# Kernel tuning notes

Measured on AMD Instinct MI355X. Metric: run time of the kernel, lower is better.

## Reference

```python
import jax, jax.numpy as jnp
import numpy as np
from jax import lax

N_CLASS = 21          # VOC: 20 foreground + background
SCORE_THRESH = 0.05   # 'evaluate' preset
NMS_THRESH = 0.3


def loc2bbox(src_bbox, loc):
    # src_bbox, loc: [N, 4] in (y1, x1, y2, x2) / (dy, dx, dh, dw)
    h = src_bbox[:, 2] - src_bbox[:, 0]
    w = src_bbox[:, 3] - src_bbox[:, 1]
    cy = src_bbox[:, 0] + 0.5 * h
    cx = src_bbox[:, 1] + 0.5 * w
    dy, dx, dh, dw = loc[:, 0], loc[:, 1], loc[:, 2], loc[:, 3]
    ncy = dy * h + cy
    ncx = dx * w + cx
    nh = jnp.exp(dh) * h
    nw = jnp.exp(dw) * w
    return jnp.stack([ncy - 0.5 * nh, ncx - 0.5 * nw,
                      ncy + 0.5 * nh, ncx + 0.5 * nw], axis=1)


def pairwise_iou(boxes):
    # boxes: [R, 4] (y1, x1, y2, x2) -> [R, R]
    area = (boxes[:, 2] - boxes[:, 0]) * (boxes[:, 3] - boxes[:, 1])
    ty1 = jnp.maximum(boxes[:, None, 0], boxes[None, :, 0])
    tx1 = jnp.maximum(boxes[:, None, 1], boxes[None, :, 1])
    ty2 = jnp.minimum(boxes[:, None, 2], boxes[None, :, 2])
    tx2 = jnp.minimum(boxes[:, None, 3], boxes[None, :, 3])
    inter = jnp.clip(ty2 - ty1, 0) * jnp.clip(tx2 - tx1, 0)
    union = area[:, None] + area[None, :] - inter
    return inter / jnp.maximum(union, 1e-10)


def nms_keep(boxes, scores):
    # boxes [R,4], scores [R] for one class. Returns bool keep mask [R]
    # (score-thresholded + greedy NMS), fixed shape (mask instead of gather).
    R = boxes.shape[0]
    valid = scores > SCORE_THRESH
    order = jnp.argsort(-scores)
    b = boxes[order]
    v = valid[order]
    suppress = pairwise_iou(b) > NMS_THRESH  # [R, R]
    idx = jnp.arange(R)

    def body(i, keep):
        sup_by_earlier = jnp.any(keep & suppress[:, i] & (idx < i))
        return keep.at[i].set(v[i] & ~sup_by_earlier)

    keep_sorted = lax.fori_loop(0, R, body, jnp.zeros((R,), bool))
    return jnp.zeros((R,), bool).at[order].set(keep_sorted)


def setup_inputs() -> dict:
    key = jax.random.key(0)
    k1, k2, k3, k4 = jax.random.split(key, 4)
    R = 2000
    size_h, size_w = 600, 800
    roi_cls_loc = jax.random.normal(k1, (R, N_CLASS * 4), jnp.float32)
    roi_scores = jax.random.normal(k2, (R, N_CLASS), jnp.float32)
    # valid (y1, x1, y2, x2) rois inside the image
    yx = jax.random.uniform(k3, (R, 2), jnp.float32) * jnp.array([size_h - 32.0, size_w - 32.0])
    hw = 16.0 + jax.random.uniform(k4, (R, 2), jnp.float32) * 128.0
    rois = jnp.concatenate([yx, yx + hw], axis=1)
    return {"roi_cls_loc": roi_cls_loc, "roi_scores": roi_scores,
            "rois": rois, "size_h": size_h, "size_w": size_w}


def reference(roi_cls_loc, roi_scores, rois, size_h, size_w):
    R = rois.shape[0]
    mean = jnp.tile(jnp.asarray([0.0, 0.0, 0.0, 0.0], roi_cls_loc.dtype), N_CLASS)
    std = jnp.tile(jnp.asarray([0.1, 0.1, 0.2, 0.2], roi_cls_loc.dtype), N_CLASS)
    loc = roi_cls_loc * std + mean                      # [R, 4*C]
    loc = loc.reshape(R * N_CLASS, 4)
    src = jnp.broadcast_to(rois[:, None, :], (R, N_CLASS, 4)).reshape(R * N_CLASS, 4)
    box = loc2bbox(src, loc).reshape(R, N_CLASS, 4)
    # clamp y coords (0,2) to [0, H], x coords (1,3) to [0, W]
    y = jnp.clip(box[..., 0::2], 0.0, float(size_h))
    x = jnp.clip(box[..., 1::2], 0.0, float(size_w))
    box = jnp.stack([y[..., 0], x[..., 0], y[..., 1], x[..., 1]], axis=-1)
    prob = jax.nn.softmax(roi_scores, axis=1)           # [R, C]
    # foreground classes only (skip background class 0)
    cls_box = jnp.transpose(box[:, 1:, :], (1, 0, 2))   # [C-1, R, 4]
    cls_prob = prob[:, 1:].T                            # [C-1, R]
    keep = jax.vmap(nms_keep)(lax.stop_gradient(cls_box),
                              lax.stop_gradient(cls_prob))  # [C-1, R] bool
    kept = keep.astype(box.dtype)[..., None]
    # fixed-shape detections: per-class boxes + score, zeroed where suppressed
    out = jnp.concatenate([cls_box * kept, cls_prob[..., None] * kept], axis=-1)
    return out  # [C-1, R, 5]
```

## Files before the change

### kernel.cpp

```cpp
#include <hip/hip_runtime.h>
#include <math.h>

#define NCLS 21
#define NCO 20
#define SUB 8
#define TPB 256
#define RCAP 2048
#define RMAX 2000
#define LDSW 7680
#define SCORE_THRESH 0.05f

typedef unsigned long long u64;
typedef unsigned int u32;
typedef unsigned short u16;

#define IOU_MID (20132661.0 / 67108864.0)

__device__ __forceinline__ u64 readlane64(u64 v, int l) {
    u32 lo = (u32)__builtin_amdgcn_readlane((int)(u32)v, l);
    u32 hi = (u32)__builtin_amdgcn_readlane((int)(u32)(v >> 32), l);
    return ((u64)hi << 32) | lo;
}
__device__ __forceinline__ float readlanef(float v, int l) {
    return __uint_as_float((u32)__builtin_amdgcn_readlane((int)__float_as_uint(v), l));
}
__device__ __forceinline__ u64 shflxor64(u64 v, int m) {
    u32 lo = (u32)__shfl_xor((int)(u32)v, m, 64);
    u32 hi = (u32)__shfl_xor((int)(u32)(v >> 32), m, 64);
    return ((u64)hi << 32) | lo;
}

__device__ __forceinline__ int coff(int ic, int nw) {
    return ((ic * nw - ((ic * (ic - 1)) >> 1)) << 6);
}

__device__ __forceinline__ void decode_box(
    const float* __restrict__ rois, const float* __restrict__ loc,
    int r, int cls, float sh, float sw,
    float& by1, float& bx1, float& by2, float& bx2)
{
    float4 rb = *(const float4*)(rois + r * 4);
    float y1 = rb.x, x1 = rb.y, y2 = rb.z, x2 = rb.w;
    float h = y2 - y1, w = x2 - x1;
    float cy = y1 + 0.5f * h, cx = x1 + 0.5f * w;
    float4 l4 = *(const float4*)(loc + r * (NCLS * 4) + cls * 4);
    float dy = l4.x * 0.1f, dx = l4.y * 0.1f;
    float dh = l4.z * 0.2f, dw = l4.w * 0.2f;
    float ncy = dy * h + cy, ncx = dx * w + cx;
    float nh = expf(dh) * h, nw = expf(dw) * w;
    by1 = fminf(fmaxf(ncy - 0.5f * nh, 0.f), sh);
    bx1 = fminf(fmaxf(ncx - 0.5f * nw, 0.f), sw);
    by2 = fminf(fmaxf(ncy + 0.5f * nh, 0.f), sh);
    bx2 = fminf(fmaxf(ncx + 0.5f * nw, 0.f), sw);
}

__device__ __forceinline__ float softmax_p(
    const float* __restrict__ scores, int r, int cls)
{
    const float* srow = scores + r * NCLS;
    float s[NCLS];
    float4 a0 = *(const float4*)(srow);
    float4 a1 = *(const float4*)(srow + 4);
    float4 a2 = *(const float4*)(srow + 8);
    float4 a3 = *(const float4*)(srow + 12);
    float4 a4 = *(const float4*)(srow + 16);
    s[0]=a0.x; s[1]=a0.y; s[2]=a0.z; s[3]=a0.w;
    s[4]=a1.x; s[5]=a1.y; s[6]=a1.z; s[7]=a1.w;
    s[8]=a2.x; s[9]=a2.y; s[10]=a2.z; s[11]=a2.w;
    s[12]=a3.x; s[13]=a3.y; s[14]=a3.z; s[15]=a3.w;
    s[16]=a4.x; s[17]=a4.y; s[18]=a4.z; s[19]=a4.w;
    s[20]=srow[20];
    float m = -INFINITY;
#pragma unroll
    for (int k = 0; k < NCLS; ++k) m = fmaxf(m, s[k]);
    float sum = 0.f, ec = 0.f;
#pragma unroll
    for (int k = 0; k < NCLS; ++k) {
        float e = expf(s[k] - m);
        sum += e;
        if (k == cls) ec = e;
    }
    return ec / sum;
}

__global__ __launch_bounds__(256) void keygen_kernel(
    const float* __restrict__ scores, u64* __restrict__ ukey,
    int* __restrict__ cntA, int R)
{
    __shared__ u64 lkey[256];
    __shared__ int cnt;
    const int t = threadIdx.x;
    const int c = blockIdx.x >> 3;
    const int s = blockIdx.x & 7;
    const int lane = t & 63;
    if (t == 0) cnt = 0;
    __syncthreads();
    const int rpb = (R + 7) >> 3;
    const int r0 = s * rpb, r1 = min(R, r0 + rpb);
    for (int r = r0 + t; r < r1; r += 256) {
        float p = softmax_p(scores, r, c + 1);
        bool valid = (p > SCORE_THRESH);
        u64 key = ((u64)(~__float_as_uint(p)) << 32) | (u32)r;
        u64 bal = __ballot(valid);
        if (bal) {
            int nb = (int)__popcll(bal);
            int base = 0;
            if (lane == 0) base = atomicAdd(&cnt, nb);
            base = __shfl(base, 0, 64);
            if (valid)
                lkey[base + (int)__popcll(bal & ((1ull << lane) - 1ull))] = key;
        }
    }
    __syncthreads();
    const int n = cnt;
    if (t == 0) cntA[(c << 3) | s] = n;
    for (int j = t; j < n; j += 256)
        ukey[((size_t)c << 11) + (s << 8) + j] = lkey[j];
}

__global__ __launch_bounds__(512) void rank_kernel(
    const float* __restrict__ loc, const float* __restrict__ rois,
    const int* __restrict__ ph, const int* __restrict__ pw,
    const u64* __restrict__ ukey, const int* __restrict__ cntA,
    u64* __restrict__ ord, int* __restrict__ nvv,
    float4* __restrict__ pbG, float* __restrict__ arG, int R)
{
    __shared__ __align__(16) u64 vkey[RCAP + 2];
    const int t = threadIdx.x;
    const int c = blockIdx.x >> 3;
    const int s = blockIdx.x & 7;
    const int wv = t >> 6, lane = t & 63;
    int nv = 0, bseg = 0, nseg = 0;
#pragma unroll
    for (int k = 0; k < 8; ++k) {
        int ck = cntA[(c << 3) | k];
        if (k < wv) bseg += ck;
        if (k == wv) nseg = ck;
        nv += ck;
    }
    for (int j = lane; j < nseg; j += 64)
        vkey[bseg + j] = ukey[((size_t)c << 11) + (wv << 8) + j];
    if (t == 0) vkey[nv] = ~0ull;
    __syncthreads();

    const int sl = (nv + 7) >> 3;
    const int i0 = s * sl;
    const int nmy = max(0, min(nv - i0, sl));
    if (t < nmy) {
        u64 kk = vkey[i0 + t];
        int rank = 0;
        const ulonglong2* vk2 = (const ulonglong2*)vkey;
        const int nj2 = (nv + 1) >> 1;
#pragma unroll 8
        for (int j = 0; j < nj2; ++j) {
            ulonglong2 kj = vk2[j];
            rank += (int)(kj.x < kk) + (int)(kj.y < kk);
        }
        const float sh = (float)(*ph), sw = (float)(*pw);
        int r = (int)(u32)kk;
        float b0, b1, b2, b3;
        decode_box(rois, loc, r, c + 1, sh, sw, b0, b1, b2, b3);
        ord[((size_t)c << 11) + rank] = kk;
        pbG[((size_t)c << 11) + rank] = make_float4(b0, b1, b2, b3);
        arG[((size_t)c << 11) + rank] = (b2 - b0) * (b3 - b1);
    }
    if (t == 0 && s == 0) nvv[c] = nv;
}

__global__ __launch_bounds__(512) void maskp_kernel(
    const float4* __restrict__ pbG, const float* __restrict__ arG,
    const int* __restrict__ nvv, u64* __restrict__ M)
{
    __shared__ float4 pb[RCAP];
    __shared__ float ar[RCAP];
    const int t = threadIdx.x;
    const int c = blockIdx.x >> 3;
    const int s = blockIdx.x & 7;
    const int lane = t & 63;
    const int nv = nvv[c];
    const int nw = (nv + 63) >> 6;
    for (int i = t; i < nv; i += 512) {
        pb[i] = pbG[((size_t)c << 11) + i];
        ar[i] = arG[((size_t)c << 11) + i];
    }
    __syncthreads();

    const int wid = (s << 3) | (t >> 6);
    const int ntasks = nw * (nw + 1) / 2;
    u64* Mc = M + ((size_t)c << 16);
    for (int task = wid; task < ntasks; task += SUB * 8) {
        int ic = 0, rm = task;
        while (rm >= nw - ic) { rm -= nw - ic; ++ic; }
        int v = ic + rm;
        int i = (ic << 6) + lane;
        float4 a = pb[i];
        float iarea = ar[i];
        float4 rj = pb[(v << 6) + lane];
        float ja_l = ar[(v << 6) + lane];
        int jcnt = min(64, nv - (v << 6));
        u64 m = 0;
        for (int jj = 0; jj < jcnt; ++jj) {
            float jy1 = readlanef(rj.x, jj);
            float jx1 = readlanef(rj.y, jj);
            float jy2 = readlanef(rj.z, jj);
            float jx2 = readlanef(rj.w, jj);
            float ja  = readlanef(ja_l, jj);
            float ty1 = fmaxf(a.x, jy1);
            float tx1 = fmaxf(a.y, jx1);
            float ty2 = fminf(a.z, jy2);
            float tx2 = fminf(a.w, jx2);
            float inter = fmaxf(ty2 - ty1, 0.f) * fmaxf(tx2 - tx1, 0.f);
            float uni = fmaxf(iarea + ja - inter, 1e-10f);
            if ((double)inter > IOU_MID * (double)uni) m |= 1ull << jj;
        }
        if (v == ic) m &= (lane < 63) ? (~0ull << (lane + 1)) : 0ull;
        int W = nw - ic;
        if (i < nv) Mc[coff(ic, nw) + lane * W + (v - ic)] = m;
    }
}

__global__ __launch_bounds__(TPB) void resolveout_kernel(
    const float* __restrict__ loc, const float* __restrict__ rois,
    const int* __restrict__ ph, const int* __restrict__ pw,
    const u64* __restrict__ ord, const int* __restrict__ nvv,
    const u64* __restrict__ M, float* __restrict__ out, int R)
{
    __shared__ u64 mlds[LDSW];
    __shared__ u64 keptw[32];
    const int t = threadIdx.x;
    const int c = blockIdx.x >> 3;
    const int s = blockIdx.x & 7;
    const int nv = nvv[c];
    const int nw = (nv + 63) >> 6;
    const u64* Mc = M + ((size_t)c << 16);
    const int S = coff(nw, nw);
    const bool lds_ok = (S <= LDSW);
    if (t < 32) keptw[t] = 0;

    if (lds_ok) {
        for (int base = 0; base < S; base += 2048) {
            u64 v[8];
#pragma unroll
            for (int j = 0; j < 8; ++j) {
                int k = base + (j << 8) + t;
                v[j] = (k < S) ? Mc[k] : 0ull;
            }
#pragma unroll
            for (int j = 0; j < 8; ++j) {
                int k = base + (j << 8) + t;
                if (k < S) mlds[k] = v[j];
            }
        }
    }
    __syncthreads();

    if (t < 64) {
        const int lane = t;
        auto core = [&](const auto* B) {
            u64 remreg = 0;
            for (int w = 0; w < nw; ++w) {
                const int W = nw - w;
                const int cb = coff(w, nw);
                int i = (w << 6) + lane;
                u64 cw = (i < nv) ? B[cb + lane * W] : 0ull;
                int remn = nv - (w << 6);
                u64 vb = (remn >= 64) ? ~0ull : ((1ull << remn) - 1ull);
                u64 cand = vb & ~readlane64(remreg, w);
                u64 X = cand;
                if (X) {
                    for (int it = 0; it < 64; ++it) {
                        u64 contrib = ((X >> lane) & 1ull) ? cw : 0ull;
#pragma unroll
                        for (int d = 1; d < 64; d <<= 1)
                            contrib |= shflxor64(contrib, d);
                        bool keep = ((cand >> lane) & 1ull) &&
                                    !((contrib >> lane) & 1ull);
                        u64 Xn = __ballot(keep);
                        if (Xn == X) break;
                        X = Xn;
                    }
                    if (lane == 0) keptw[w] = X;
                    bool lact = (lane > w) && (lane < nw);
                    u64 km = X, acc = 0;
                    while (km) {
                        int bs[8];
#pragma unroll
                        for (int g = 0; g < 8; ++g) {
                            bs[g] = km ? (__ffsll(km) - 1) : -1;
                            if (km) km &= km - 1;
                        }
                        u64 tmp[8];
#pragma unroll
                        for (int g = 0; g < 8; ++g)
                            tmp[g] = (bs[g] >= 0 && lact)
                                ? B[cb + bs[g] * W + (lane - w)] : 0ull;
#pragma unroll
                        for (int g = 0; g < 8; ++g) acc |= tmp[g];
                    }
                    if (lact) remreg |= acc;
                }
            }
        };
        if (lds_ok) core(mlds); else core(Mc);
    }
    __syncthreads();

    const int chunk = (R + 7) >> 3;
    const int r0 = s * chunk;
    const int r1 = min(R, r0 + chunk);
    float* slice = out + (size_t)c * R * 5;
    for (int k = r0 * 5 + t; k < r1 * 5; k += TPB) slice[k] = 0.f;
    __syncthreads();

    const float sh = (float)(*ph), sw = (float)(*pw);
    for (int i = t; i < nv; i += TPB) {
        if ((keptw[i >> 6] >> (i & 63)) & 1ull) {
            u64 key = ord[((size_t)c << 11) + i];
            int r = (int)(u32)key;
            if (r >= r0 && r < r1) {
                float v0, v1, v2, v3;
                decode_box(rois, loc, r, c + 1, sh, sw, v0, v1, v2, v3);
                float* p = slice + (size_t)r * 5;
                p[0] = v0; p[1] = v1; p[2] = v2; p[3] = v3;
                p[4] = __uint_as_float(~(u32)(key >> 32));
            }
        }
    }
}

#define NTH 1024
__global__ __launch_bounds__(NTH) void fused_kernel(
    const float* __restrict__ loc, const float* __restrict__ scores,
    const float* __restrict__ rois, const int* __restrict__ ph,
    const int* __restrict__ pw, float* __restrict__ out, int R)
{
    __shared__ u64 vkey[RMAX];
    __shared__ float2 p1[RMAX], p2[RMAX];
    __shared__ u64 chunk[64 * 33];
    __shared__ u64 rem[32];
    __shared__ int cnt;

    const int t = threadIdx.x;
    const int lane = t & 63;
    const int c = blockIdx.x + 1;
    const float sh = (float)(*ph), sw = (float)(*pw);

    if (t == 0) cnt = 0;
    if (t < 32) rem[t] = 0;
    __syncthreads();

    for (int r = t; r < R; r += NTH) {
        float p = softmax_p(scores, r, c);
        if (p > SCORE_THRESH) {
            int j = atomicAdd(&cnt, 1);
            vkey[j] = ((u64)(~__float_as_uint(p)) << 32) | (u32)r;
        }
    }
    __syncthreads();
    const int nv = cnt;
    const int nw = (nv + 63) >> 6;

    u64 kk0 = 0, kk1 = 0;
    int r0 = 0, r1 = 0;
    bool in0 = (t < nv), in1 = (t + NTH < nv);
    if (in0) kk0 = vkey[t];
    if (in1) kk1 = vkey[t + NTH];
#pragma unroll 8
    for (int i = 0; i < nv; ++i) {
        u64 k = vkey[i];
        r0 += (k < kk0);
        r1 += (k < kk1);
    }
    __syncthreads();

    for (int u = 0; u < 2; ++u) {
        bool act = u ? in1 : in0;
        if (act) {
            u64 kk = u ? kk1 : kk0;
            int rank = u ? r1 : r0;
            int r = (int)(kk & 0xffffffffu);
            float b0, b1, b2, b3;
            decode_box(rois, loc, r, c, sh, sw, b0, b1, b2, b3);
            vkey[rank] = kk;
            p1[rank] = make_float2(b0, b1);
            p2[rank] = make_float2(b2, b3);
        }
    }
    __syncthreads();

    for (int w = 0; w < nw; ++w) {
        int nwr = nw - w;
        u64 remw = rem[w];
        for (int task = t; task < (nwr << 6); task += NTH) {
            int vr = task >> 6, il = task & 63;
            int i = (w << 6) + il;
            u64 m = 0;
            if (i < nv && !((remw >> il) & 1ull)) {
                int v = w + vr;
                u64 rv = rem[v];
                if (~rv != 0ull) {
                    float2 a1 = p1[i], a2 = p2[i];
                    float iarea = (a2.x - a1.x) * (a2.y - a1.y);
                    int j0 = v << 6;
                    int jhi = min(64, nv - j0);
#pragma unroll 4
                    for (int jj = 0; jj < jhi; ++jj) {
                        float2 b1 = p1[j0 + jj], b2 = p2[j0 + jj];
                        float ty1 = fmaxf(a1.x, b1.x);
                        float tx1 = fmaxf(a1.y, b1.y);
                        float ty2 = fminf(a2.x, b2.x);
                        float tx2 = fminf(a2.y, b2.y);
                        float inter = fmaxf(ty2 - ty1, 0.f) * fmaxf(tx2 - tx1, 0.f);
                        float jarea = (b2.x - b1.x) * (b2.y - b1.y);
                        float uni = fmaxf(iarea + jarea - inter, 1e-10f);
                        if ((double)inter > IOU_MID * (double)uni) m |= 1ull << jj;
                    }
                    if (vr == 0)
                        m &= (il < 63) ? (~0ull << (il + 1)) : 0ull;
                }
            }
            chunk[il * 33 + vr] = m;
        }
        __syncthreads();

        u64 cand = chunk[lane * 33];
        u64 cur = rem[w];
        int remn = nv - (w << 6);
        u64 vb = (remn >= 64) ? ~0ull : ((1ull << remn) - 1ull);
        u64 avail = vb & ~cur;
        u64 kept = 0;
        while (avail) {
            int bb = __ffsll(avail) - 1;
            kept |= 1ull << bb;
            cur |= __shfl(cand, bb, 64);
            avail &= ~(cur | (1ull << bb));
        }
        int vr = t & 31, pg = t >> 5;
        if (vr >= 1 && vr < nwr) {
            u64 acc = 0, km = kept;
            int n = 0;
            while (km) {
                int bb = __ffsll(km) - 1;
                km &= km - 1;
                if ((n & 31) == pg) acc |= chunk[bb * 33 + vr];
                ++n;
            }
            if (acc) atomicOr(&rem[w + vr], acc);
        }
        if (t == 0) rem[w] = cur;
        __syncthreads();
    }

    u16* inv = (u16*)chunk;
    for (int r = t; r < R; r += NTH) inv[r] = 0xffffu;
    __syncthreads();
    for (int i = t; i < nv; i += NTH)
        if (!((rem[i >> 6] >> (i & 63)) & 1ull))
            inv[(int)(vkey[i] & 0xffffffffu)] = (u16)i;
    __syncthreads();
    float* slice = out + (size_t)(c - 1) * R * 5;
    for (int r = t; r < R; r += NTH) {
        int i = inv[r];
        float v0 = 0.f, v1 = 0.f, v2 = 0.f, v3 = 0.f, v4 = 0.f;
        if (i != 0xffff) {
            float2 a1 = p1[i], a2 = p2[i];
            v0 = a1.x; v1 = a1.y; v2 = a2.x; v3 = a2.y;
            v4 = __uint_as_float(~(u32)(vkey[i] >> 32));
        }
        float* p = slice + (size_t)r * 5;
        p[0] = v0; p[1] = v1; p[2] = v2; p[3] = v3; p[4] = v4;
    }
}

extern "C" void kernel_launch(void* const* d_in, const int* in_sizes, int n_in,
                              void* d_out, int out_size, void* d_ws, size_t ws_size,
                              hipStream_t stream) {
    const float* loc    = (const float*)d_in[0];
    const float* scores = (const float*)d_in[1];
    const float* rois   = (const float*)d_in[2];
    const int*   ph     = (const int*)d_in[3];
    const int*   pw     = (const int*)d_in[4];
    float* out = (float*)d_out;
    int R = in_sizes[2] / 4;

    size_t needM    = (size_t)NCO * RCAP * 32 * 8;
    size_t needOrd  = (size_t)NCO * RCAP * 8;
    size_t needUkey = (size_t)NCO * RCAP * 8;
    size_t needPbG  = (size_t)NCO * RCAP * 16;
    size_t needArG  = (size_t)NCO * RCAP * 4;
    size_t need     = needM + needOrd + needUkey + needPbG + needArG + 2048;

    if (R <= RCAP && ws_size >= need) {
        char* w     = (char*)d_ws;
        u64* M      = (u64*)w;                               w += needM;
        u64* ordp   = (u64*)w;                               w += needOrd;
        u64* ukey   = (u64*)w;                               w += needUkey;
        float4* pbG = (float4*)w;                            w += needPbG;
        float* arG  = (float*)w;                             w += needArG;
        int* cntA   = (int*)w;                               w += 1024;
        int* nvv    = (int*)w;
        keygen_kernel<<<NCO * SUB, 256, 0, stream>>>(scores, ukey, cntA, R);
        rank_kernel<<<NCO * SUB, 512, 0, stream>>>(loc, rois, ph, pw, ukey,
                                                   cntA, ordp, nvv, pbG, arG, R);
        maskp_kernel<<<NCO * SUB, 512, 0, stream>>>(pbG, arG, nvv, M);
        resolveout_kernel<<<NCO * SUB, TPB, 0, stream>>>(loc, rois, ph, pw,
                                                         ordp, nvv, M, out, R);
    } else if (R <= RMAX) {
        fused_kernel<<<NCO, NTH, 0, stream>>>(loc, scores, rois, ph, pw, out, R);
    }
}
```

Measured before the change: 116.8 us.

## Raise per-class block count to 12 and split rank counting across four lanes

Raises the number of blocks per class from 8 to 12 in all four kernels, generalising segment indexing for keys and counts. The rank kernel now gives each key four threads, each counting over a quarter of the key array, and combines them with xor shuffles, which shortens the serial compare loop. The aim is more parallelism on a GPU with many compute units and less per-thread latency in ranking. The cost is more blocks that each redo the shared-memory loads (LDS fill in maskp, matrix load in resolveout), plus a new R <= 3072 limit on the fast path.

```diff
diff --git a/kernel.cpp b/kernel.cpp
--- a/kernel.cpp
+++ b/kernel.cpp
@@ -3,10 +3,11 @@
 
 #define NCLS 21
 #define NCO 20
-#define SUB 8
+#define SUB 12
 #define TPB 256
 #define RCAP 2048
 #define RMAX 2000
+#define SEGW 256
 #define LDSW 7680
 #define SCORE_THRESH 0.05f
 
@@ -83,21 +84,21 @@
     return ec / sum;
 }
 
-__global__ __launch_bounds__(256) void keygen_kernel(
+__global__ __launch_bounds__(TPB) void keygen_kernel(
     const float* __restrict__ scores, u64* __restrict__ ukey,
     int* __restrict__ cntA, int R)
 {
-    __shared__ u64 lkey[256];
+    __shared__ u64 lkey[TPB];
     __shared__ int cnt;
     const int t = threadIdx.x;
-    const int c = blockIdx.x >> 3;
-    const int s = blockIdx.x & 7;
+    const int c = blockIdx.x / SUB;
+    const int s = blockIdx.x % SUB;
     const int lane = t & 63;
     if (t == 0) cnt = 0;
     __syncthreads();
-    const int rpb = (R + 7) >> 3;
+    const int rpb = (R + SUB - 1) / SUB;
     const int r0 = s * rpb, r1 = min(R, r0 + rpb);
-    for (int r = r0 + t; r < r1; r += 256) {
+    for (int r = r0 + t; r < r1; r += TPB) {
         float p = softmax_p(scores, r, c + 1);
         bool valid = (p > SCORE_THRESH);
         u64 key = ((u64)(~__float_as_uint(p)) << 32) | (u32)r;
@@ -113,9 +114,9 @@
     }
     __syncthreads();
     const int n = cnt;
-    if (t == 0) cntA[(c << 3) | s] = n;
-    for (int j = t; j < n; j += 256)
-        ukey[((size_t)c << 11) + (s << 8) + j] = lkey[j];
+    if (t == 0) cntA[(c << 4) | s] = n;
+    for (int j = t; j < n; j += TPB)
+        ukey[(size_t)c * (SUB * SEGW) + s * SEGW + j] = lkey[j];
 }
 
 __global__ __launch_bounds__(512) void rank_kernel(
@@ -127,42 +128,55 @@
 {
     __shared__ __align__(16) u64 vkey[RCAP + 2];
     const int t = threadIdx.x;
-    const int c = blockIdx.x >> 3;
-    const int s = blockIdx.x & 7;
+    const int c = blockIdx.x / SUB;
+    const int s = blockIdx.x % SUB;
     const int wv = t >> 6, lane = t & 63;
-    int nv = 0, bseg = 0, nseg = 0;
-#pragma unroll
-    for (int k = 0; k < 8; ++k) {
-        int ck = cntA[(c << 3) | k];
-        if (k < wv) bseg += ck;
-        if (k == wv) nseg = ck;
+    int nv = 0;
+    int baseA = 0, nA = 0, baseB = 0, nB = 0;
+#pragma unroll
+    for (int k = 0; k < SUB; ++k) {
+        int ck = cntA[(c << 4) | k];
+        if (k < wv)     baseA += ck;
+        if (k == wv)    nA = ck;
+        if (k < wv + 8) baseB += ck;
+        if (k == wv + 8) nB = ck;
         nv += ck;
     }
-    for (int j = lane; j < nseg; j += 64)
-        vkey[bseg + j] = ukey[((size_t)c << 11) + (wv << 8) + j];
+    for (int j = lane; j < nA; j += 64)
+        vkey[baseA + j] = ukey[(size_t)c * (SUB * SEGW) + wv * SEGW + j];
+    if (wv + 8 < SUB)
+        for (int j = lane; j < nB; j += 64)
+            vkey[baseB + j] = ukey[(size_t)c * (SUB * SEGW) + (wv + 8) * SEGW + j];
     if (t == 0) vkey[nv] = ~0ull;
     __syncthreads();
 
-    const int sl = (nv + 7) >> 3;
+    const int sl = (nv + SUB - 1) / SUB;
     const int i0 = s * sl;
     const int nmy = max(0, min(nv - i0, sl));
-    if (t < nmy) {
-        u64 kk = vkey[i0 + t];
+    const int q = t & 3;
+    const ulonglong2* vk2 = (const ulonglong2*)vkey;
+    const int nj2 = (nv + 1) >> 1;
+    const int jb0 = (q * nj2) >> 2;
+    const int jb1 = ((q + 1) * nj2) >> 2;
+    const float shf = (float)(*ph), swf = (float)(*pw);
+    for (int il = (t >> 2); il < nmy; il += 128) {
+        u64 kk = vkey[i0 + il];
         int rank = 0;
-        const ulonglong2* vk2 = (const ulonglong2*)vkey;
-        const int nj2 = (nv + 1) >> 1;
 #pragma unroll 8
-        for (int j = 0; j < nj2; ++j) {
+        for (int j = jb0; j < jb1; ++j) {
             ulonglong2 kj = vk2[j];
             rank += (int)(kj.x < kk) + (int)(kj.y < kk);
         }
-        const float sh = (float)(*ph), sw = (float)(*pw);
-        int r = (int)(u32)kk;
-        float b0, b1, b2, b3;
-        decode_box(rois, loc, r, c + 1, sh, sw, b0, b1, b2, b3);
-        ord[((size_t)c << 11) + rank] = kk;
-        pbG[((size_t)c << 11) + rank] = make_float4(b0, b1, b2, b3);
-        arG[((size_t)c << 11) + rank] = (b2 - b0) * (b3 - b1);
+        rank += __shfl_xor(rank, 1, 64);
+        rank += __shfl_xor(rank, 2, 64);
+        if (q == 0) {
+            int r = (int)(u32)kk;
+            float b0, b1, b2, b3;
+            decode_box(rois, loc, r, c + 1, shf, swf, b0, b1, b2, b3);
+            ord[((size_t)c << 11) + rank] = kk;
+            pbG[((size_t)c << 11) + rank] = make_float4(b0, b1, b2, b3);
+            arG[((size_t)c << 11) + rank] = (b2 - b0) * (b3 - b1);
+        }
     }
     if (t == 0 && s == 0) nvv[c] = nv;
 }
@@ -174,8 +188,8 @@
     __shared__ float4 pb[RCAP];
     __shared__ float ar[RCAP];
     const int t = threadIdx.x;
-    const int c = blockIdx.x >> 3;
-    const int s = blockIdx.x & 7;
+    const int c = blockIdx.x / SUB;
+    const int s = blockIdx.x % SUB;
     const int lane = t & 63;
     const int nv = nvv[c];
     const int nw = (nv + 63) >> 6;
@@ -228,8 +242,8 @@
     __shared__ u64 mlds[LDSW];
     __shared__ u64 keptw[32];
     const int t = threadIdx.x;
-    const int c = blockIdx.x >> 3;
-    const int s = blockIdx.x & 7;
+    const int c = blockIdx.x / SUB;
+    const int s = blockIdx.x % SUB;
     const int nv = nvv[c];
     const int nw = (nv + 63) >> 6;
     const u64* Mc = M + ((size_t)c << 16);
@@ -305,7 +319,7 @@
     }
     __syncthreads();
 
-    const int chunk = (R + 7) >> 3;
+    const int chunk = (R + SUB - 1) / SUB;
     const int r0 = s * chunk;
     const int r1 = min(R, r0 + chunk);
     float* slice = out + (size_t)c * R * 5;
@@ -485,21 +499,22 @@
 
     size_t needM    = (size_t)NCO * RCAP * 32 * 8;
     size_t needOrd  = (size_t)NCO * RCAP * 8;
-    size_t needUkey = (size_t)NCO * RCAP * 8;
+    size_t needUkey = (size_t)NCO * SUB * SEGW * 8;
     size_t needPbG  = (size_t)NCO * RCAP * 16;
     size_t needArG  = (size_t)NCO * RCAP * 4;
-    size_t need     = needM + needOrd + needUkey + needPbG + needArG + 2048;
-
-    if (R <= RCAP && ws_size >= need) {
+    size_t need     = needM + needOrd + needUkey + needPbG + needArG + 4096;
+
+    if (R <= RCAP && R <= SUB * SEGW && ws_size >= need) {
         char* w     = (char*)d_ws;
         u64* M      = (u64*)w;                               w += needM;
         u64* ordp   = (u64*)w;                               w += needOrd;
         u64* ukey   = (u64*)w;                               w += needUkey;
         float4* pbG = (float4*)w;                            w += needPbG;
         float* arG  = (float*)w;                             w += needArG;
-        int* cntA   = (int*)w;                               w += 1024;
+        int* cntA   = (int*)w;                               w += 2048;
         int* nvv    = (int*)w;
-        keygen_kernel<<<NCO * SUB, 256, 0, stream>>>(scores, ukey, cntA, R);
+
+        keygen_kernel<<<NCO * SUB, TPB, 0, stream>>>(scores, ukey, cntA, R);
         rank_kernel<<<NCO * SUB, 512, 0, stream>>>(loc, rois, ph, pw, ukey,
                                                    cntA, ordp, nvv, pbG, arG, R);
         maskp_kernel<<<NCO * SUB, 512, 0, stream>>>(pbG, arG, nvv, M);
```

Result: faster. 111.3 us, median of 2 (-4.7%).
